# Performance work log

Measured on AMD Instinct MI355X. Metric: run time of the kernel, lower is better.

The kernel has to match this reference:

```python
import jax, jax.numpy as jnp
import numpy as np
import math

B, T, C, NH, NL, AD, V, BS, MT = 32, 50, 128, 8, 6, 64, 18, 150, 4096
HD = C // NH


def setup_inputs():
    key = jax.random.key(0)
    ks = jax.random.split(key, 32)
    w = lambda i, shape, s=0.02: (jax.random.normal(ks[i], shape) * s).astype(jnp.float32)
    d = {}
    d["states"] = jax.random.uniform(ks[0], (B, T, 4, 84, 84), jnp.float32)
    d["rtgs"] = jax.random.normal(ks[1], (B, T, 1), jnp.float32)
    d["actions"] = jax.random.randint(ks[2], (B, T, 1), 0, V)
    d["timesteps"] = jax.random.randint(ks[3], (B, 1, 1), 0, MT)
    d["targets"] = jax.random.randint(ks[4], (B, T, 1), 0, V)
    d["pos_emb"] = w(5, (1, BS + 1, C))
    d["global_pos_emb"] = w(6, (1, MT + 1, C))
    d["c1_w"] = w(7, (32, 4, 8, 8)); d["c1_b"] = w(8, (32,), 0.01)
    d["c2_w"] = w(9, (64, 32, 4, 4)); d["c2_b"] = w(10, (64,), 0.01)
    d["c3_w"] = w(11, (64, 64, 3, 3)); d["c3_b"] = w(12, (64,), 0.01)
    d["enc_w"] = w(13, (C, 3136)); d["enc_b"] = w(14, (C,), 0.01)
    d["ret_w"] = w(15, (C, 1)); d["ret_b"] = w(16, (C,), 0.01)
    d["act_tab"] = w(17, (V, C))
    d["ln_w"] = jnp.ones((NL, 3, C), jnp.float32)
    d["ln_b"] = jnp.zeros((NL, 3, C), jnp.float32)
    d["attn_w"] = w(18, (NL, 4, C, C)); d["attn_b"] = w(19, (NL, 4, C), 0.01)
    d["mlp_w1"] = w(20, (NL, 4 * C, C)); d["mlp_b1"] = w(21, (NL, 4 * C), 0.01)
    d["mlp_w2"] = w(22, (NL, C, 4 * C)); d["mlp_b2"] = w(23, (NL, C), 0.01)
    d["ad_dw"] = w(24, (NL, AD, C), 1e-3); d["ad_db"] = jnp.zeros((NL, AD), jnp.float32)
    d["ad_uw"] = w(25, (NL, C, AD), 1e-3); d["ad_ub"] = jnp.zeros((NL, C), jnp.float32)
    d["lnf_w"] = jnp.ones((C,), jnp.float32); d["lnf_b"] = jnp.zeros((C,), jnp.float32)
    d["head_w"] = w(26, (V, C))
    return d


def _ln(x, g, b):
    m = jnp.mean(x, -1, keepdims=True)
    v = jnp.mean(jnp.square(x - m), -1, keepdims=True)
    return (x - m) * jax.lax.rsqrt(v + 1e-5) * g + b


def _conv(x, w, b, s):
    y = jax.lax.conv_general_dilated(x, w, (s, s), "VALID", dimension_numbers=("NCHW", "OIHW", "NCHW"))
    return y + b[None, :, None, None]


def _forward(states, rtgs, pos_emb, global_pos_emb, c1_w, c1_b, c2_w, c2_b, c3_w, c3_b,
             enc_w, enc_b, ret_w, ret_b, act_tab, ln_w, ln_b, attn_w, attn_b,
             mlp_w1, mlp_b1, mlp_w2, mlp_b2, ad_dw, ad_db, ad_uw, ad_ub,
             lnf_w, lnf_b, head_w, actions, timesteps):
    # state encoder (conv stem): [B*T,4,84,84] -> [B,T,C]
    x = states.reshape(-1, 4, 84, 84)
    x = jax.nn.relu(_conv(x, c1_w, c1_b, 4))  # -> 20x20
    x = jax.nn.relu(_conv(x, c2_w, c2_b, 2))  # -> 9x9
    x = jax.nn.relu(_conv(x, c3_w, c3_b, 1))  # -> 7x7
    x = x.reshape(x.shape[0], -1)             # 64*7*7 = 3136
    state_e = jnp.tanh(x @ enc_w.T + enc_b).reshape(B, T, C)
    rtg_e = jnp.tanh(rtgs @ ret_w.T + ret_b)
    act_e = jnp.tanh(act_tab[actions[..., 0]])
    # interleave rtg/state/action at [::3],[1::3],[2::3]
    tok = jnp.stack([rtg_e, state_e, act_e], axis=2).reshape(B, 3 * T, C)
    S = 3 * T
    pe = global_pos_emb[0][timesteps[:, 0, 0]][:, None, :] + pos_emb[:, :S, :]
    h = tok + pe  # drop = identity in eval
    mask = jnp.tril(jnp.ones((S, S), bool))
    scale = 1.0 / math.sqrt(HD)
    for l in range(NL):
        normed = _ln(h, ln_w[l, 2], ln_b[l, 2])           # ln3 on pre-block input
        xa = _ln(h, ln_w[l, 0], ln_b[l, 0])               # ln1
        k = (xa @ attn_w[l, 0].T + attn_b[l, 0]).reshape(B, S, NH, HD)
        q = (xa @ attn_w[l, 1].T + attn_b[l, 1]).reshape(B, S, NH, HD)
        v = (xa @ attn_w[l, 2].T + attn_b[l, 2]).reshape(B, S, NH, HD)
        att = jnp.einsum("bihd,bjhd->bhij", q, k) * scale
        att = jax.nn.softmax(jnp.where(mask, att, -jnp.inf), axis=-1)
        y = jnp.einsum("bhij,bjhd->bihd", att, v).reshape(B, S, C)
        h1 = h + y @ attn_w[l, 3].T + attn_b[l, 3]
        xm = _ln(h1, ln_w[l, 1], ln_b[l, 1])              # ln2
        f = h1 + jax.nn.gelu(xm @ mlp_w1[l].T + mlp_b1[l], approximate=False) @ mlp_w2[l].T + mlp_b2[l]
        ad = jax.nn.relu(normed @ ad_dw[l].T + ad_db[l]) @ ad_uw[l].T + ad_ub[l]
        h = h1 + f + ad                                   # x = hidden + drop(forward) + adapter
    logits = _ln(h, lnf_w, lnf_b) @ head_w.T
    return logits[:, 1::3, :]  # predictions from state tokens


def reference(states, rtgs, pos_emb, global_pos_emb, c1_w, c1_b, c2_w, c2_b, c3_w, c3_b,
              enc_w, enc_b, ret_w, ret_b, act_tab, ln_w, ln_b, attn_w, attn_b,
              mlp_w1, mlp_b1, mlp_w2, mlp_b2, ad_dw, ad_db, ad_uw, ad_ub,
              lnf_w, lnf_b, head_w, actions, timesteps, targets):
    # targets only toggles sequence layout (not None here) and the CE loss; logits are the kernel payload
    return _forward(states, rtgs, pos_emb, global_pos_emb, c1_w, c1_b, c2_w, c2_b, c3_w, c3_b,
                    enc_w, enc_b, ret_w, ret_b, act_tab, ln_w, ln_b, attn_w, attn_b,
                    mlp_w1, mlp_b1, mlp_w2, mlp_b2, ad_dw, ad_db, ad_uw, ad_ub,
                    lnf_w, lnf_b, head_w, actions, timesteps)
```

## Files before the change

kernel.cpp:

```cpp
#include <hip/hip_runtime.h>
#include <hip/hip_bf16.h>
#include <math.h>

typedef __hip_bfloat16 bf16;

typedef __attribute__((ext_vector_type(8))) short bfrag;
typedef __attribute__((ext_vector_type(4))) float f32x4;
union FragU { bfrag s; uint2 d[2]; unsigned int u[4]; };

static __device__ __forceinline__ float b2f(bf16 x){ return __bfloat162float(x); }
static __device__ __forceinline__ float2 upk2(unsigned int u){
  union { unsigned int i; float f; } a, b;
  a.i = u << 16;
  b.i = u & 0xffff0000u;
  float2 r; r.x = a.f; r.y = b.f; return r;
}
static __device__ __forceinline__ unsigned int f2b2(float lo, float hi){
  bf16 l = __float2bfloat16(lo), h = __float2bfloat16(hi);
  unsigned short lb, hb;
  __builtin_memcpy(&lb, &l, 2); __builtin_memcpy(&hb, &h, 2);
  return (unsigned int)lb | ((unsigned int)hb << 16);
}
static __device__ __forceinline__ void sto(float* p, size_t i, float v){ p[i] = v; }
static __device__ __forceinline__ void sto(bf16* p, size_t i, float v){ p[i] = __float2bfloat16(v); }

constexpr size_t MiB = 1ull << 20;
constexpr size_t OFF_C1   = 0;
constexpr size_t OFF_C2   = 41*MiB;
constexpr size_t OFF_C3   = 58*MiB;
constexpr size_t OFF_SE   = 69*MiB;
constexpr size_t OFF_H    = 0;
constexpr size_t OFF_XA   = 3*MiB;
constexpr size_t OFF_NORM = 6*MiB;
constexpr size_t OFF_QKV  = 9*MiB;
constexpr size_t OFF_Y    = 17*MiB;
constexpr size_t OFF_H1   = 20*MiB;
constexpr size_t OFF_MLPH = 23*MiB;
constexpr size_t OFF_ADH  = 33*MiB;

__global__ __launch_bounds__(256) void conv1_kernel(
    const float* __restrict__ x, const float* __restrict__ w,
    const float* __restrict__ bias, bf16* __restrict__ out)
{
  __shared__ bf16 xs1[4*84*88];
  int b = blockIdx.x;
  int t = threadIdx.x;
  const float4* xb4 = (const float4*)(x + (size_t)b*28224);
  for (int e = t; e < 7056; e += 256){
    int c = e / 1764, rem = e % 1764;
    int r = rem / 21, c4 = (rem % 21)*4;
    float4 f = xb4[e];
    *(uint2*)(xs1 + (c*84 + r)*88 + c4) = make_uint2(f2b2(f.x, f.y), f2b2(f.z, f.w));
  }
  __syncthreads();
  int lane = t & 63, wave = t >> 6;
  int quad = lane >> 4, r16 = lane & 15;
  f32x4 acc[7][2];
  #pragma unroll
  for (int i = 0; i < 7; ++i)
    #pragma unroll
    for (int j = 0; j < 2; ++j) acc[i][j] = (f32x4){0.f,0.f,0.f,0.f};
  for (int kc = 0; kc < 8; ++kc){
    int c = kc >> 1, ky = (kc & 1)*4 + quad;
    FragU bf_[2];
    #pragma unroll
    for (int tn = 0; tn < 2; ++tn){
      int oc = tn*16 + r16;
      const float* wp = w + oc*256 + kc*32 + quad*8;
      float4 wa = ((const float4*)wp)[0], wb = ((const float4*)wp)[1];
      bf_[tn].u[0] = f2b2(wa.x, wa.y); bf_[tn].u[1] = f2b2(wa.z, wa.w);
      bf_[tn].u[2] = f2b2(wb.x, wb.y); bf_[tn].u[3] = f2b2(wb.z, wb.w);
    }
    #pragma unroll
    for (int i = 0; i < 7; ++i){
      int tile = wave*7 + i;
      if (tile < 25){
        int m = tile*16 + r16;
        int oy = m / 20, ox = m % 20;
        const bf16* p = xs1 + ((c*84 + 4*oy + ky)*88 + 4*ox);
        FragU a;
        a.d[0] = *(const uint2*)p;
        a.d[1] = *(const uint2*)(p + 4);
        acc[i][0] = __builtin_amdgcn_mfma_f32_16x16x32_bf16(a.s, bf_[0].s, acc[i][0], 0, 0, 0);
        acc[i][1] = __builtin_amdgcn_mfma_f32_16x16x32_bf16(a.s, bf_[1].s, acc[i][1], 0, 0, 0);
      }
    }
  }
  __syncthreads();
  #pragma unroll
  for (int i = 0; i < 7; ++i){
    int tile = wave*7 + i;
    if (tile < 25){
      int m0 = tile*16 + quad*4;
      #pragma unroll
      for (int tn = 0; tn < 2; ++tn){
        int oc = tn*16 + r16;
        float bb = bias[oc];
        float v0 = fmaxf(acc[i][tn][0] + bb, 0.f);
        float v1 = fmaxf(acc[i][tn][1] + bb, 0.f);
        float v2 = fmaxf(acc[i][tn][2] + bb, 0.f);
        float v3 = fmaxf(acc[i][tn][3] + bb, 0.f);
        *(uint2*)(xs1 + oc*408 + m0) = make_uint2(f2b2(v0, v1), f2b2(v2, v3));
      }
    }
  }
  __syncthreads();
  bf16* outp = out + (size_t)b*12800;
  for (int e = t; e < 1600; e += 256){
    int oc = e / 50, col = e % 50;
    uint4 v = *(const uint4*)(xs1 + oc*408 + col*8);
    *(uint4*)(outp + oc*400 + col*8) = v;
  }
}

__global__ __launch_bounds__(256) void conv2_kernel(
    const bf16* __restrict__ x, const float* __restrict__ w,
    const float* __restrict__ bias, bf16* __restrict__ out)
{
  __shared__ bf16 xs2[32*20*24];
  int b = blockIdx.x;
  int t = threadIdx.x;
  const unsigned int* xb = (const unsigned int*)(x + (size_t)b*12800);
  for (int p = t; p < 6400; p += 256){
    int c = p / 200, rem = p % 200;
    int r = rem / 10, cp = rem % 10;
    ((unsigned int*)xs2)[((c*20 + r)*24 + 2*cp) >> 1] = xb[p];
  }
  __syncthreads();
  int lane = t & 63, wave = t >> 6;
  int quad = lane >> 4, r16 = lane & 15;
  int oc = wave*16 + r16;
  f32x4 acc[6];
  #pragma unroll
  for (int i = 0; i < 6; ++i) acc[i] = (f32x4){0.f,0.f,0.f,0.f};
  for (int kc = 0; kc < 16; ++kc){
    const float* wp = w + oc*512 + kc*32 + quad*8;
    float4 wa = ((const float4*)wp)[0], wb = ((const float4*)wp)[1];
    FragU bfr;
    bfr.u[0] = f2b2(wa.x, wa.y); bfr.u[1] = f2b2(wa.z, wa.w);
    bfr.u[2] = f2b2(wb.x, wb.y); bfr.u[3] = f2b2(wb.z, wb.w);
    int c = kc*2 + (quad >> 1);
    int ky0 = (quad & 1)*2;
    #pragma unroll
    for (int tile = 0; tile < 6; ++tile){
      int m = tile*16 + r16; if (m > 80) m = 80;
      int oy = m / 9, ox = m % 9;
      int idx1 = (c*20 + 2*oy + ky0)*24 + 2*ox;
      const unsigned int* q1 = (const unsigned int*)(xs2 + idx1);
      const unsigned int* q2 = (const unsigned int*)(xs2 + idx1 + 24);
      FragU a;
      a.u[0] = q1[0]; a.u[1] = q1[1];
      a.u[2] = q2[0]; a.u[3] = q2[1];
      acc[tile] = __builtin_amdgcn_mfma_f32_16x16x32_bf16(a.s, bfr.s, acc[tile], 0, 0, 0);
    }
  }
  __syncthreads();
  float bb = bias[oc];
  #pragma unroll
  for (int tile = 0; tile < 6; ++tile){
    #pragma unroll
    for (int r = 0; r < 4; ++r){
      int m = tile*16 + quad*4 + r;
      if (m < 81){
        float v = fmaxf(acc[tile][r] + bb, 0.f);
        xs2[oc*81 + m] = __float2bfloat16(v);
      }
    }
  }
  __syncthreads();
  const unsigned int* lsu = (const unsigned int*)xs2;
  unsigned int* op = (unsigned int*)(out + (size_t)b*5184);
  for (int e = t; e < 2592; e += 256) op[e] = lsu[e];
}

__global__ __launch_bounds__(256) void conv3_kernel(
    const bf16* __restrict__ x, const float* __restrict__ w,
    const float* __restrict__ bias, bf16* __restrict__ out)
{
  __shared__ float xsf[5184];
  int b = blockIdx.x;
  int t = threadIdx.x;
  const bf16* xb = x + (size_t)b*5184;
  for (int e = t; e < 2592; e += 256){
    unsigned int u = *(const unsigned int*)(xb + 2*e);
    float2 f = upk2(u);
    xsf[2*e] = f.x; xsf[2*e+1] = f.y;
  }
  __syncthreads();
  int oc = t & 63;
  int oy1 = t >> 6;
  bool two = (t < 192);
  float a1[7] = {}, a2[7] = {};
  const float* wb3 = w + oc*576;
  for (int c = 0; c < 64; ++c){
    #pragma unroll
    for (int ky = 0; ky < 3; ++ky){
      const float* wp = wb3 + c*9 + ky*3;
      float w0 = wp[0], w1 = wp[1], w2 = wp[2];
      const float* r1 = xsf + c*81 + (oy1+ky)*9;
      #pragma unroll
      for (int ox = 0; ox < 7; ++ox) a1[ox] += r1[ox]*w0 + r1[ox+1]*w1 + r1[ox+2]*w2;
      if (two){
        const float* r2 = xsf + c*81 + (oy1+4+ky)*9;
        #pragma unroll
        for (int ox = 0; ox < 7; ++ox) a2[ox] += r2[ox]*w0 + r2[ox+1]*w1 + r2[ox+2]*w2;
      }
    }
  }
  float bb = bias[oc];
  size_t o1 = (size_t)b*3136 + oc*49 + oy1*7;
  #pragma unroll
  for (int ox = 0; ox < 7; ++ox) out[o1+ox] = __float2bfloat16(fmaxf(a1[ox]+bb, 0.f));
  if (two){
    size_t o2 = (size_t)b*3136 + oc*49 + (oy1+4)*7;
    #pragma unroll
    for (int ox = 0; ox < 7; ++ox) out[o2+ox] = __float2bfloat16(fmaxf(a2[ox]+bb, 0.f));
  }
}

template<int ACT, typename OT>
__global__ __launch_bounds__(256) void mgemm(
    const bf16* __restrict__ X, const float* __restrict__ W,
    const float* __restrict__ bias, const float* __restrict__ add, float add_scale,
    OT* __restrict__ out, int M, int N, int K)
{
  __shared__ bf16 Xs[64*40];
  __shared__ bf16 Ws[64*40];
  int nb = N >> 6;
  int bn = (blockIdx.x % nb) << 6;
  int bm = (blockIdx.x / nb) << 6;
  int t = threadIdx.x;
  int lane = t & 63, wave = t >> 6;
  int mw = wave >> 1, nw = wave & 1;
  int quad = lane >> 4, r16 = lane & 15;
  int srow = t >> 2, scol = (t & 3)*8;
  f32x4 acc[2][2];
  #pragma unroll
  for (int i = 0; i < 2; ++i)
    #pragma unroll
    for (int j = 0; j < 2; ++j) acc[i][j] = (f32x4){0.f,0.f,0.f,0.f};
  for (int k0 = 0; k0 < K; k0 += 32){
    uint4 xv = *(const uint4*)(X + (size_t)(bm + srow)*K + k0 + scol);
    uint2* xd = (uint2*)(Xs + srow*40 + scol);
    xd[0] = make_uint2(xv.x, xv.y); xd[1] = make_uint2(xv.z, xv.w);
    const float* wp = W + (size_t)(bn + srow)*K + k0 + scol;
    float4 wa = ((const float4*)wp)[0], wb = ((const float4*)wp)[1];
    uint2* wd = (uint2*)(Ws + srow*40 + scol);
    wd[0] = make_uint2(f2b2(wa.x, wa.y), f2b2(wa.z, wa.w));
    wd[1] = make_uint2(f2b2(wb.x, wb.y), f2b2(wb.z, wb.w));
    __syncthreads();
    FragU af[2], bf_[2];
    #pragma unroll
    for (int tm = 0; tm < 2; ++tm){
      const bf16* p = Xs + (mw*32 + tm*16 + r16)*40 + quad*8;
      af[tm].d[0] = *(const uint2*)p; af[tm].d[1] = *(const uint2*)(p + 4);
    }
    #pragma unroll
    for (int tn = 0; tn < 2; ++tn){
      const bf16* p = Ws + (nw*32 + tn*16 + r16)*40 + quad*8;
      bf_[tn].d[0] = *(const uint2*)p; bf_[tn].d[1] = *(const uint2*)(p + 4);
    }
    #pragma unroll
    for (int tm = 0; tm < 2; ++tm)
      #pragma unroll
      for (int tn = 0; tn < 2; ++tn)
        acc[tm][tn] = __builtin_amdgcn_mfma_f32_16x16x32_bf16(af[tm].s, bf_[tn].s, acc[tm][tn], 0, 0, 0);
    __syncthreads();
  }
  #pragma unroll
  for (int tm = 0; tm < 2; ++tm){
    #pragma unroll
    for (int tn = 0; tn < 2; ++tn){
      int n = bn + nw*32 + tn*16 + r16;
      float bb = bias[n];
      #pragma unroll
      for (int r = 0; r < 4; ++r){
        int m = bm + mw*32 + tm*16 + quad*4 + r;
        float v = acc[tm][tn][r] + bb;
        if (ACT == 1) v = tanhf(v);
        else if (ACT == 2) v = 0.5f*v*(1.0f + erff(v*0.70710678118f));
        else if (ACT == 3) v = fmaxf(v, 0.f);
        if (add) v += add_scale * add[(size_t)m*N + n];
        sto(out, (size_t)m*N + n, v);
      }
    }
  }
}

__global__ __launch_bounds__(256) void token_kernel(
    const float* __restrict__ rtgs, const int* __restrict__ actions, const int* __restrict__ timesteps,
    const float* __restrict__ ret_w, const float* __restrict__ ret_b, const float* __restrict__ act_tab,
    const float* __restrict__ pos_emb, const float* __restrict__ gpe,
    const float* __restrict__ se, float* __restrict__ h)
{
  int idx = blockIdx.x*256 + threadIdx.x;
  int c = idx & 127; int row = idx >> 7;
  int s = row % 150; int b = row / 150;
  int t = s / 3; int r = s - 3*t;
  float tok;
  if (r == 0)      tok = tanhf(rtgs[b*50+t] * ret_w[c] + ret_b[c]);
  else if (r == 1) tok = se[(b*50+t)*128 + c];
  else             tok = tanhf(act_tab[actions[b*50+t]*128 + c]);
  float pe = gpe[(size_t)timesteps[b]*128 + c] + pos_emb[s*128 + c];
  h[idx] = tok + pe;
}

__global__ __launch_bounds__(256) void ln_kernel(
    const float* __restrict__ x,
    const float* __restrict__ g1, const float* __restrict__ be1, bf16* __restrict__ o1,
    const float* __restrict__ g2, const float* __restrict__ be2, bf16* o2)
{
  int lane = threadIdx.x & 63;
  int row = blockIdx.x*4 + (threadIdx.x >> 6);
  const float2 xv = *(const float2*)(x + (size_t)row*128 + lane*2);
  float s = xv.x + xv.y, sq = xv.x*xv.x + xv.y*xv.y;
  #pragma unroll
  for (int off = 32; off; off >>= 1){ s += __shfl_xor(s, off); sq += __shfl_xor(sq, off); }
  float mean = s * 0.0078125f;
  float var  = sq * 0.0078125f - mean*mean;
  float rstd = rsqrtf(var + 1e-5f);
  float n0 = (xv.x - mean)*rstd, n1 = (xv.y - mean)*rstd;
  int c0 = lane*2;
  ((unsigned int*)o1)[row*64 + lane] = f2b2(n0*g1[c0] + be1[c0], n1*g1[c0+1] + be1[c0+1]);
  if (o2)
    ((unsigned int*)o2)[row*64 + lane] = f2b2(n0*g2[c0] + be2[c0], n1*g2[c0+1] + be2[c0+1]);
}

__global__ __launch_bounds__(256) void attn_kernel(const bf16* __restrict__ qkv, bf16* __restrict__ y)
{
  int bh = blockIdx.x;
  int hh = bh & 7; int b = bh >> 3;
  __shared__ float ks[150*16];
  __shared__ float vs[150*16];
  int t = threadIdx.x;
  for (int i = t; i < 2400; i += 256){
    int s = i >> 4; int d = i & 15;
    const bf16* base = qkv + (size_t)(b*150 + s)*384;
    ks[i] = b2f(base[hh*16 + d]);
    vs[i] = b2f(base[256 + hh*16 + d]);
  }
  __syncthreads();
  if (t < 150){
    const bf16* qr = qkv + (size_t)(b*150 + t)*384 + 128 + hh*16;
    float q[16];
    #pragma unroll
    for (int d = 0; d < 16; ++d) q[d] = b2f(qr[d]) * 0.25f;
    float m = -1e30f, l = 0.f, acc[16] = {};
    for (int j = 0; j <= t; ++j){
      const float* kr = ks + j*16;
      float s = 0.f;
      #pragma unroll
      for (int d = 0; d < 16; ++d) s += q[d]*kr[d];
      float mn = fmaxf(m, s);
      float corr = __expf(m - mn);
      float p = __expf(s - mn);
      l = l*corr + p;
      const float* vr = vs + j*16;
      #pragma unroll
      for (int d = 0; d < 16; ++d) acc[d] = acc[d]*corr + p*vr[d];
      m = mn;
    }
    float inv = 1.f / l;
    bf16* yr = y + (size_t)(b*150 + t)*128 + hh*16;
    #pragma unroll
    for (int d = 0; d < 16; ++d) yr[d] = __float2bfloat16(acc[d]*inv);
  }
}

__global__ __launch_bounds__(64) void head_kernel(
    const float* __restrict__ h, const float* __restrict__ g, const float* __restrict__ be,
    const float* __restrict__ hw, float* __restrict__ out)
{
  int bt = blockIdx.x;
  int lane = threadIdx.x;
  int b = bt / 50, t = bt % 50;
  const float* row = h + ((size_t)b*150 + 3*t + 1)*128;
  float2 xv = *(const float2*)(row + lane*2);
  float s = xv.x + xv.y, sq = xv.x*xv.x + xv.y*xv.y;
  #pragma unroll
  for (int off = 32; off; off >>= 1){ s += __shfl_xor(s, off); sq += __shfl_xor(sq, off); }
  float mean = s * 0.0078125f;
  float var  = sq * 0.0078125f - mean*mean;
  float rstd = rsqrtf(var + 1e-5f);
  int c0 = lane*2;
  __shared__ float sh[128];
  sh[c0]   = (xv.x-mean)*rstd*g[c0]   + be[c0];
  sh[c0+1] = (xv.y-mean)*rstd*g[c0+1] + be[c0+1];
  __syncthreads();
  if (lane < 18){
    const float* wr = hw + lane*128;
    float acc = 0.f;
    #pragma unroll
    for (int c = 0; c < 128; c += 4){
      float4 wf = *(const float4*)(wr + c);
      acc += sh[c]*wf.x + sh[c+1]*wf.y + sh[c+2]*wf.z + sh[c+3]*wf.w;
    }
    out[bt*18 + lane] = acc;
  }
}

extern "C" void kernel_launch(void* const* d_in, const int* in_sizes, int n_in,
                              void* d_out, int out_size, void* d_ws, size_t ws_size,
                              hipStream_t stream)
{
  const float* states    = (const float*)d_in[0];
  const float* rtgs      = (const float*)d_in[1];
  const int*   actions   = (const int*)d_in[2];
  const int*   timesteps = (const int*)d_in[3];
  const float* pos_emb   = (const float*)d_in[5];
  const float* gpe       = (const float*)d_in[6];
  const float* c1_w = (const float*)d_in[7];  const float* c1_b = (const float*)d_in[8];
  const float* c2_w = (const float*)d_in[9];  const float* c2_b = (const float*)d_in[10];
  const float* c3_w = (const float*)d_in[11]; const float* c3_b = (const float*)d_in[12];
  const float* enc_w = (const float*)d_in[13]; const float* enc_b = (const float*)d_in[14];
  const float* ret_w = (const float*)d_in[15]; const float* ret_b = (const float*)d_in[16];
  const float* act_tab = (const float*)d_in[17];
  const float* ln_w = (const float*)d_in[18]; const float* ln_b = (const float*)d_in[19];
  const float* attn_w = (const float*)d_in[20]; const float* attn_b = (const float*)d_in[21];
  const float* mlp_w1 = (const float*)d_in[22]; const float* mlp_b1 = (const float*)d_in[23];
  const float* mlp_w2 = (const float*)d_in[24]; const float* mlp_b2 = (const float*)d_in[25];
  const float* ad_dw = (const float*)d_in[26]; const float* ad_db = (const float*)d_in[27];
  const float* ad_uw = (const float*)d_in[28]; const float* ad_ub = (const float*)d_in[29];
  const float* lnf_w = (const float*)d_in[30]; const float* lnf_b = (const float*)d_in[31];
  const float* head_w = (const float*)d_in[32];
  float* out = (float*)d_out;

  char* ws = (char*)d_ws;
  bf16* c1o  = (bf16*)(ws + OFF_C1);
  bf16* c2o  = (bf16*)(ws + OFF_C2);
  bf16* c3o  = (bf16*)(ws + OFF_C3);
  float* se  = (float*)(ws + OFF_SE);
  float* h   = (float*)(ws + OFF_H);
  bf16* xa   = (bf16*)(ws + OFF_XA);
  bf16* nrm  = (bf16*)(ws + OFF_NORM);
  bf16* qkv  = (bf16*)(ws + OFF_QKV);
  bf16* y    = (bf16*)(ws + OFF_Y);
  float* h1  = (float*)(ws + OFF_H1);
  bf16* mlph = (bf16*)(ws + OFF_MLPH);
  bf16* adh  = (bf16*)(ws + OFF_ADH);

  conv1_kernel<<<1600, 256, 0, stream>>>(states, c1_w, c1_b, c1o);
  conv2_kernel<<<1600, 256, 0, stream>>>(c1o, c2_w, c2_b, c2o);
  conv3_kernel<<<1600, 256, 0, stream>>>(c2o, c3_w, c3_b, c3o);
  mgemm<1, float><<<25*2, 256, 0, stream>>>(c3o, enc_w, enc_b, nullptr, 0.f, se, 1600, 128, 3136);
  token_kernel<<<2400, 256, 0, stream>>>(rtgs, actions, timesteps, ret_w, ret_b, act_tab,
                                         pos_emb, gpe, se, h);

  for (int l = 0; l < 6; ++l){
    const float* g1 = ln_w + (l*3+0)*128; const float* be1 = ln_b + (l*3+0)*128;
    const float* g2 = ln_w + (l*3+1)*128; const float* be2 = ln_b + (l*3+1)*128;
    const float* g3 = ln_w + (l*3+2)*128; const float* be3 = ln_b + (l*3+2)*128;
    ln_kernel<<<1200, 256, 0, stream>>>(h, g1, be1, xa, g3, be3, nrm);
    mgemm<0, bf16><<<75*6, 256, 0, stream>>>(xa, attn_w + (size_t)l*4*16384, attn_b + l*4*128,
                                             nullptr, 0.f, qkv, 4800, 384, 128);
    attn_kernel<<<256, 256, 0, stream>>>(qkv, y);
    mgemm<0, float><<<75*2, 256, 0, stream>>>(y, attn_w + ((size_t)l*4+3)*16384, attn_b + (l*4+3)*128,
                                              h, 1.0f, h1, 4800, 128, 128);
    ln_kernel<<<1200, 256, 0, stream>>>(h1, g2, be2, xa, nullptr, nullptr, nullptr);
    mgemm<2, bf16><<<75*8, 256, 0, stream>>>(xa, mlp_w1 + (size_t)l*65536, mlp_b1 + l*512,
                                             nullptr, 0.f, mlph, 4800, 512, 128);
    mgemm<3, bf16><<<75*1, 256, 0, stream>>>(nrm, ad_dw + (size_t)l*8192, ad_db + l*64,
                                             nullptr, 0.f, adh, 4800, 64, 128);
    mgemm<0, float><<<75*2, 256, 0, stream>>>(mlph, mlp_w2 + (size_t)l*65536, mlp_b2 + l*128,
                                              h1, 2.0f, h, 4800, 128, 512);
    mgemm<0, float><<<75*2, 256, 0, stream>>>(adh, ad_uw + (size_t)l*8192, ad_ub + l*128,
                                              h, 1.0f, h, 4800, 128, 64);
  }
  head_kernel<<<1600, 64, 0, stream>>>(h, lnf_w, lnf_b, head_w, out);
}
```

Before: 1.245 ms.

## Rewrite conv3 as implicit GEMM on bf16 MFMA with pre-transposed weights

Replaces the scalar fp32 direct 3x3 convolution in conv3 with an implicit-GEMM formulation using 16x16x32 bf16 MFMA instructions. Input activations are transposed in shared memory to position-major layout. A new small kernel converts the conv3 weights to bf16 in tap-major order, writing into workspace offset 0 (the conv1 output region, which is dead by then). This trades scalar FMA throughput for matrix-core throughput, at the cost of an extra launch, the transpose pass, and bf16 weight precision.

Measured after the change: 1.109 ms. 1.12x faster.

```diff
diff --git a/kernel.cpp b/kernel.cpp
--- a/kernel.cpp
+++ b/kernel.cpp
@@ -37,6 +37,7 @@
 constexpr size_t OFF_H1   = 20*MiB;
 constexpr size_t OFF_MLPH = 23*MiB;
 constexpr size_t OFF_ADH  = 33*MiB;
+constexpr size_t OFF_WT   = 0;
 
 __global__ __launch_bounds__(256) void conv1_kernel(
     const float* __restrict__ x, const float* __restrict__ w,
@@ -173,49 +174,74 @@
   for (int e = t; e < 2592; e += 256) op[e] = lsu[e];
 }
 
+__global__ __launch_bounds__(256) void wt_kernel(const float* __restrict__ w, bf16* __restrict__ wt)
+{
+  int o = blockIdx.x*256 + threadIdx.x;
+  int oc = o / 576, r = o % 576;
+  int tap = r >> 6, c = r & 63;
+  wt[o] = __float2bfloat16(w[oc*576 + c*9 + tap]);
+}
+
 __global__ __launch_bounds__(256) void conv3_kernel(
-    const bf16* __restrict__ x, const float* __restrict__ w,
+    const bf16* __restrict__ x, const bf16* __restrict__ wt,
     const float* __restrict__ bias, bf16* __restrict__ out)
 {
-  __shared__ float xsf[5184];
+  __shared__ ushort lin[5184];
+  __shared__ ushort xt[81*72];
   int b = blockIdx.x;
   int t = threadIdx.x;
-  const bf16* xb = x + (size_t)b*5184;
-  for (int e = t; e < 2592; e += 256){
-    unsigned int u = *(const unsigned int*)(xb + 2*e);
-    float2 f = upk2(u);
-    xsf[2*e] = f.x; xsf[2*e+1] = f.y;
-  }
-  __syncthreads();
-  int oc = t & 63;
-  int oy1 = t >> 6;
-  bool two = (t < 192);
-  float a1[7] = {}, a2[7] = {};
-  const float* wb3 = w + oc*576;
-  for (int c = 0; c < 64; ++c){
-    #pragma unroll
-    for (int ky = 0; ky < 3; ++ky){
-      const float* wp = wb3 + c*9 + ky*3;
-      float w0 = wp[0], w1 = wp[1], w2 = wp[2];
-      const float* r1 = xsf + c*81 + (oy1+ky)*9;
-      #pragma unroll
-      for (int ox = 0; ox < 7; ++ox) a1[ox] += r1[ox]*w0 + r1[ox+1]*w1 + r1[ox+2]*w2;
-      if (two){
-        const float* r2 = xsf + c*81 + (oy1+4+ky)*9;
-        #pragma unroll
-        for (int ox = 0; ox < 7; ++ox) a2[ox] += r2[ox]*w0 + r2[ox+1]*w1 + r2[ox+2]*w2;
+  const uint2* xb = (const uint2*)(x + (size_t)b*5184);
+  for (int i = t; i < 1296; i += 256) ((uint2*)lin)[i] = xb[i];
+  __syncthreads();
+  for (int e = t; e < 5184; e += 256){
+    int c = e & 63, p = e >> 6;
+    xt[p*72 + c] = lin[c*81 + p];
+  }
+  __syncthreads();
+  int lane = t & 63, wv = t >> 6;
+  int quad = lane >> 4, r16 = lane & 15;
+  int m = wv*16 + r16;
+  int pos = m < 49 ? m : 48;
+  int pb = (pos/7)*9 + (pos%7);
+  const ushort* abase = xt + pb*72 + quad*8;
+  const bf16* wb0 = wt + (size_t)r16*576 + quad*8;
+  f32x4 acc[4];
+  #pragma unroll
+  for (int tn = 0; tn < 4; ++tn) acc[tn] = (f32x4){0.f,0.f,0.f,0.f};
+  #pragma unroll 3
+  for (int kc = 0; kc < 18; ++kc){
+    int tap = kc >> 1;
+    int toff = (tap/3)*9 + (tap%3);
+    int soff = toff*72 + (kc & 1)*32;
+    FragU a;
+    uint4 av = *(const uint4*)(abase + soff);
+    a.u[0] = av.x; a.u[1] = av.y; a.u[2] = av.z; a.u[3] = av.w;
+    #pragma unroll
+    for (int tn = 0; tn < 4; ++tn){
+      uint4 bv = *(const uint4*)(wb0 + tn*9216 + kc*32);
+      FragU bfr;
+      bfr.u[0] = bv.x; bfr.u[1] = bv.y; bfr.u[2] = bv.z; bfr.u[3] = bv.w;
+      acc[tn] = __builtin_amdgcn_mfma_f32_16x16x32_bf16(a.s, bfr.s, acc[tn], 0, 0, 0);
+    }
+  }
+  __syncthreads();
+  #pragma unroll
+  for (int tn = 0; tn < 4; ++tn){
+    int oc = tn*16 + r16;
+    float bb = bias[oc];
+    #pragma unroll
+    for (int r = 0; r < 4; ++r){
+      int p = wv*16 + quad*4 + r;
+      if (p < 49){
+        bf16 v = __float2bfloat16(fmaxf(acc[tn][r] + bb, 0.f));
+        ushort u; __builtin_memcpy(&u, &v, 2);
+        lin[oc*49 + p] = u;
       }
     }
   }
-  float bb = bias[oc];
-  size_t o1 = (size_t)b*3136 + oc*49 + oy1*7;
-  #pragma unroll
-  for (int ox = 0; ox < 7; ++ox) out[o1+ox] = __float2bfloat16(fmaxf(a1[ox]+bb, 0.f));
-  if (two){
-    size_t o2 = (size_t)b*3136 + oc*49 + (oy1+4)*7;
-    #pragma unroll
-    for (int ox = 0; ox < 7; ++ox) out[o2+ox] = __float2bfloat16(fmaxf(a2[ox]+bb, 0.f));
-  }
+  __syncthreads();
+  uint2* op = (uint2*)(out + (size_t)b*3136);
+  for (int e = t; e < 784; e += 256) op[e] = ((const uint2*)lin)[e];
 }
 
 template<int ACT, typename OT>
@@ -438,10 +464,12 @@
   float* h1  = (float*)(ws + OFF_H1);
   bf16* mlph = (bf16*)(ws + OFF_MLPH);
   bf16* adh  = (bf16*)(ws + OFF_ADH);
+  bf16* wtb  = (bf16*)(ws + OFF_WT);
 
   conv1_kernel<<<1600, 256, 0, stream>>>(states, c1_w, c1_b, c1o);
   conv2_kernel<<<1600, 256, 0, stream>>>(c1o, c2_w, c2_b, c2o);
-  conv3_kernel<<<1600, 256, 0, stream>>>(c2o, c3_w, c3_b, c3o);
+  wt_kernel<<<144, 256, 0, stream>>>(c3_w, wtb);
+  conv3_kernel<<<1600, 256, 0, stream>>>(c2o, wtb, c3_b, c3o);
   mgemm<1, float><<<25*2, 256, 0, stream>>>(c3o, enc_w, enc_b, nullptr, 0.f, se, 1600, 128, 3136);
   token_kernel<<<2400, 256, 0, stream>>>(rtgs, actions, timesteps, ret_w, ret_b, act_tab,
                                          pos_emb, gpe, se, h);
```
